# Performance work log

Measured on AMD Instinct MI355X. Metric: run time of the kernel, lower is better.

The kernel has to match this reference:

```python
import jax, jax.numpy as jnp
import numpy as np
from functools import partial

DIM, HID, DK, NH, SEQ, B = 1024, 512, 512, 4, 16, 2048
DH = DK // NH  # per-head dim = 128
EPS = 1e-5


def _ln(x, g, b):
    m = x.mean(-1, keepdims=True)
    v = ((x - m) ** 2).mean(-1, keepdims=True)
    return (x - m) * jax.lax.rsqrt(v + EPS) * g + b


def setup_inputs() -> dict:
    key = jax.random.key(0)
    ks = jax.random.split(key, 32)
    it = iter(range(32))
    n = lambda shape, s: jax.random.normal(ks[next(it)], shape, jnp.float32) * s
    inp = {
        'visual': n((B, SEQ, DIM), 1.0),
        'text':   n((B, SEQ, DIM), 1.0),
        'user':   n((B, SEQ, DIM), 1.0),
        'cat':    n((B, SEQ, DIM), 1.0),
        'label':  n((B, SEQ, 1), 1.0),
        'h0':     n((B, HID), 1.0),
        'c0':     n((B, HID), 1.0),
        # fusion MLP: Linear(4*dim -> dim)
        'fus_W': n((DIM, 4 * DIM), 1.0 / np.sqrt(4 * DIM)),
        'fus_b': n((DIM,), 0.01),
        # LayerNormLSTM cell params (gate order i,f,g,o)
        'W_ih': n((4 * HID, DIM), 1.0 / np.sqrt(DIM)),
        'W_hh': n((4 * HID, HID), 1.0 / np.sqrt(HID)),
        'g_ih': 1.0 + n((4 * HID,), 0.1), 'b_ih': n((4 * HID,), 0.01),
        'g_hh': 1.0 + n((4 * HID,), 0.1), 'b_hh': n((4 * HID,), 0.01),
        'g_c':  1.0 + n((HID,), 0.1),     'b_c':  n((HID,), 0.01),
        # attention projections
        'wq_W': n((DK, HID), 1.0 / np.sqrt(HID)), 'wq_b': n((DK,), 0.01),
        'wk_W': n((DK, HID), 1.0 / np.sqrt(HID)), 'wk_b': n((DK,), 0.01),
        'wv_W': n((NH, DK, HID), 1.0 / np.sqrt(HID)), 'wv_b': n((NH, DK), 0.01),
        'wout_W': n((DK, DK * NH), 1.0 / np.sqrt(DK * NH)), 'wout_b': n((DK,), 0.01),
        'out_W': n((1, DK), 1.0 / np.sqrt(DK)), 'out_b': n((1,), 0.01),
    }
    return inp


def reference(visual, text, user, cat, label, h0, c0, fus_W, fus_b,
              W_ih, W_hh, g_ih, b_ih, g_hh, b_hh, g_c, b_c,
              wq_W, wq_b, wk_W, wk_b, wv_W, wv_b, wout_W, wout_b, out_W, out_b):
    # fusion MLP (dropout is identity at inference)
    mods = jnp.concatenate([visual, text, user, cat], axis=-1)  # [B,S,4*DIM]
    v_t = jax.nn.relu(mods @ fus_W.T + fus_b)                    # [B,S,DIM]

    # LayerNorm-LSTM recurrence over time via scan
    def step(carry, x_t):
        h, c = carry
        gates = _ln(x_t @ W_ih.T, g_ih, b_ih) + _ln(h @ W_hh.T, g_hh, b_hh)
        i, f, g, o = jnp.split(gates, 4, axis=-1)
        c = jax.nn.sigmoid(f) * c + jax.nn.sigmoid(i) * jnp.tanh(g)
        h = jax.nn.sigmoid(o) * jnp.tanh(_ln(c, g_c, b_c))
        return (h, c), h

    (hn, _), hs = jax.lax.scan(step, (h0, c0), jnp.swapaxes(v_t, 0, 1))
    lstm_out = jnp.swapaxes(hs, 0, 1)  # [B,S,HID]

    # multi-head dot self-attention against final hidden state
    q = (hn @ wq_W.T + wq_b).reshape(-1, NH, DH)                    # [B,H,dh]
    k = (lstm_out @ wk_W.T + wk_b).reshape(-1, SEQ, NH, DH)         # [B,S,H,dh]
    scores = jnp.einsum('bshd,bhd->bhs', k, q) / np.sqrt(DH)        # [B,H,S]
    attn = jax.nn.softmax(scores, axis=-1)
    # per-head full-width values: V[b,h,s,k]
    V = jnp.einsum('hkd,bsd->bhsk', wv_W, lstm_out) + wv_b[None, :, None, :]
    ctx = jnp.einsum('bhsk,bhs->bhk', V, attn).reshape(-1, NH * DK)  # [B,H*DK]
    out_h = ctx @ wout_W.T + wout_b                                  # [B,DK]
    output = out_h @ out_W.T + out_b                                 # [B,1]

    label_one = label[:, -1, 0]
    loss = jnp.mean((output.reshape(-1) - label_one) ** 2)
    return loss, output
```

## Files before the change

kernel.cpp:

```cpp
#include <hip/hip_runtime.h>
#include <cstdint>

#define B_SZ 2048
#define SEQ  16
#define DIM  1024
#define HID  512
#define DK   512
#define NH   4
#define DH   128
#define GATE 2048
#define EPSV 1e-5f

typedef __bf16 bf8_t __attribute__((ext_vector_type(8)));
typedef float  f4_t  __attribute__((ext_vector_type(4)));
typedef unsigned short u16x8 __attribute__((ext_vector_type(8)));
typedef unsigned short u16x4 __attribute__((ext_vector_type(4)));

__device__ __forceinline__ unsigned short f2bf(float f){
  __bf16 h = (__bf16)f;
  return __builtin_bit_cast(unsigned short, h);
}
__device__ __forceinline__ float bf2f(unsigned short u){
  return __builtin_bit_cast(float, ((unsigned int)u) << 16);
}
__device__ __forceinline__ float sigm(float x){ return 1.f/(1.f+__expf(-x)); }
__device__ __forceinline__ float tanh_f(float x){ return 1.f - 2.f/(__expf(2.f*x)+1.f); }

__device__ __forceinline__ void gload16(const void* g, void* l){
  __builtin_amdgcn_global_load_lds(
      (const __attribute__((address_space(1))) void*)g,
      (__attribute__((address_space(3))) void*)l, 16, 0, 0);
}

template<bool OUT_BF16, bool BIAS, bool RELU>
__global__ __launch_bounds__(256) void gemm16(
    const unsigned short* __restrict__ A,
    const unsigned short* __restrict__ Bw,
    const float* __restrict__ bias,
    void* __restrict__ Cp,
    int N, int K, int nwg)
{
  __shared__ __align__(16) unsigned short As[128*64];
  __shared__ __align__(16) unsigned short Bs[128*64];
  const int tid = threadIdx.x, lane = tid & 63, wave = tid >> 6;
  const int bid = blockIdx.x;
  const int swz = (bid & 7)*(nwg >> 3) + (bid >> 3);
  const int nx  = N >> 7;
  const int lnx = 31 - __clz(nx);
  const int bm0 = (swz >> lnx) << 7;
  const int bn0 = (swz & (nx-1)) << 7;

  const int r8  = lane >> 3;
  const int gsw = ((lane & 7) ^ r8) * 8;
  const unsigned short* Ab = A  + (size_t)(bm0 + wave*32 + r8)*K + gsw;
  const unsigned short* Bb = Bw + (size_t)(bn0 + wave*32 + r8)*K + gsw;
  unsigned short* la = As + wave*2048;
  unsigned short* lb = Bs + wave*2048;

  f4_t acc[4][4];
  #pragma unroll
  for (int m=0;m<4;++m)
    #pragma unroll
    for (int n=0;n<4;++n) acc[m][n] = (f4_t)0.f;

  const int KT = K >> 6;
  const int fr = lane & 15, kg = lane >> 4;
  const int wm = (wave & 1)*64, wn = (wave >> 1)*64;

  for (int kt = 0; kt < KT; ++kt){
    if (kt) __syncthreads();
    const size_t ko = (size_t)kt*64;
    #pragma unroll
    for (int q = 0; q < 4; ++q){
      gload16(Ab + ko + (size_t)q*8*K, la + q*512);
      gload16(Bb + ko + (size_t)q*8*K, lb + q*512);
    }
    __syncthreads();
    #pragma unroll
    for (int kk = 0; kk < 2; ++kk){
      bf8_t af[4], bf_[4];
      #pragma unroll
      for (int m=0;m<4;++m){
        const int r = wm+m*16+fr;
        af[m]  = *(const bf8_t*)&As[r*64 + (((kk*4+kg) ^ (r&7))*8)];
      }
      #pragma unroll
      for (int n=0;n<4;++n){
        const int r = wn+n*16+fr;
        bf_[n] = *(const bf8_t*)&Bs[r*64 + (((kk*4+kg) ^ (r&7))*8)];
      }
      #pragma unroll
      for (int m=0;m<4;++m)
        #pragma unroll
        for (int n=0;n<4;++n)
          acc[m][n] = __builtin_amdgcn_mfma_f32_16x16x32_bf16(af[m], bf_[n], acc[m][n], 0,0,0);
    }
  }

  #pragma unroll
  for (int n=0;n<4;++n){
    const int col = bn0 + wn + n*16 + fr;
    float bv = 0.f;
    if constexpr (BIAS) bv = bias[col];
    #pragma unroll
    for (int m=0;m<4;++m){
      #pragma unroll
      for (int j=0;j<4;++j){
        const int row = bm0 + wm + m*16 + kg*4 + j;
        float v = acc[m][n][j] + bv;
        if constexpr (RELU) v = fmaxf(v, 0.f);
        if constexpr (OUT_BF16) ((unsigned short*)Cp)[(size_t)row*N + col] = f2bf(v);
        else                    ((float*)Cp)[(size_t)row*N + col] = v;
      }
    }
  }
}

template<bool OUT_BF16, bool BIAS>
__global__ __launch_bounds__(256) void gemm64(
    const unsigned short* __restrict__ A,
    const unsigned short* __restrict__ Bw,
    const float* __restrict__ bias,
    void* __restrict__ Cp,
    int N, int K, int nwg)
{
  __shared__ __align__(16) unsigned short As[64*64];
  __shared__ __align__(16) unsigned short Bs[64*64];
  const int tid = threadIdx.x, lane = tid & 63, wave = tid >> 6;
  const int bid = blockIdx.x;
  const int swz = (bid & 7)*(nwg >> 3) + (bid >> 3);
  const int nx  = N >> 6;
  const int lnx = 31 - __clz(nx);
  const int bm0 = (swz >> lnx) << 6;
  const int bn0 = (swz & (nx-1)) << 6;

  const int r8  = lane >> 3;
  const int gsw = ((lane & 7) ^ r8) * 8;
  const unsigned short* Ab = A  + (size_t)(bm0 + wave*16 + r8)*K + gsw;
  const unsigned short* Bb = Bw + (size_t)(bn0 + wave*16 + r8)*K + gsw;
  unsigned short* la = As + wave*1024;
  unsigned short* lb = Bs + wave*1024;

  f4_t acc[2][2];
  #pragma unroll
  for (int m=0;m<2;++m)
    #pragma unroll
    for (int n=0;n<2;++n) acc[m][n] = (f4_t)0.f;

  const int KT = K >> 6;
  const int fr = lane & 15, kg = lane >> 4;
  const int wm = (wave & 1)*32, wn = (wave >> 1)*32;

  for (int kt = 0; kt < KT; ++kt){
    if (kt) __syncthreads();
    const size_t ko = (size_t)kt*64;
    #pragma unroll
    for (int q = 0; q < 2; ++q){
      gload16(Ab + ko + (size_t)q*8*K, la + q*512);
      gload16(Bb + ko + (size_t)q*8*K, lb + q*512);
    }
    __syncthreads();
    #pragma unroll
    for (int kk = 0; kk < 2; ++kk){
      bf8_t af[2], bf_[2];
      #pragma unroll
      for (int m=0;m<2;++m){
        const int r = wm+m*16+fr;
        af[m]  = *(const bf8_t*)&As[r*64 + (((kk*4+kg) ^ (r&7))*8)];
      }
      #pragma unroll
      for (int n=0;n<2;++n){
        const int r = wn+n*16+fr;
        bf_[n] = *(const bf8_t*)&Bs[r*64 + (((kk*4+kg) ^ (r&7))*8)];
      }
      #pragma unroll
      for (int m=0;m<2;++m)
        #pragma unroll
        for (int n=0;n<2;++n)
          acc[m][n] = __builtin_amdgcn_mfma_f32_16x16x32_bf16(af[m], bf_[n], acc[m][n], 0,0,0);
    }
  }

  #pragma unroll
  for (int n=0;n<2;++n){
    const int col = bn0 + wn + n*16 + fr;
    float bv = 0.f;
    if constexpr (BIAS) bv = bias[col];
    #pragma unroll
    for (int m=0;m<2;++m){
      #pragma unroll
      for (int j=0;j<4;++j){
        const int row = bm0 + wm + m*16 + kg*4 + j;
        float v = acc[m][n][j] + bv;
        if constexpr (OUT_BF16) ((unsigned short*)Cp)[(size_t)row*N + col] = f2bf(v);
        else                    ((float*)Cp)[(size_t)row*N + col] = v;
      }
    }
  }
}

__global__ __launch_bounds__(256) void lstm_step(
  const unsigned short* __restrict__ X, const unsigned short* __restrict__ Gh,
  const float* __restrict__ c_src, float* __restrict__ c_dst,
  const float* __restrict__ g_ih, const float* __restrict__ b_ih,
  const float* __restrict__ g_hh, const float* __restrict__ b_hh,
  const float* __restrict__ g_c,  const float* __restrict__ b_c,
  unsigned short* __restrict__ h_out, unsigned short* __restrict__ lstm_out,
  int t)
{
  const int b = blockIdx.x, tid = threadIdx.x;
  __shared__ float xs[GATE];
  __shared__ float gs[GATE];
  __shared__ float red[32];
  const unsigned short* xrow = X  + ((size_t)b*SEQ + t)*GATE;
  const unsigned short* grow = Gh + (size_t)b*GATE;
  u16x8 xv = *(const u16x8*)&xrow[tid*8];
  u16x8 gv = *(const u16x8*)&grow[tid*8];
  float sx=0,sx2=0,sg=0,sg2=0;
  #pragma unroll
  for (int j=0;j<8;++j){
    float x = bf2f(xv[j]), g = bf2f(gv[j]);
    xs[tid*8+j]=x; gs[tid*8+j]=g;
    sx += x; sx2 += x*x; sg += g; sg2 += g*g;
  }
  #pragma unroll
  for (int m=32;m;m>>=1){
    sx += __shfl_xor(sx,m); sx2 += __shfl_xor(sx2,m);
    sg += __shfl_xor(sg,m); sg2 += __shfl_xor(sg2,m);
  }
  const int w = tid>>6;
  if ((tid&63)==0){ red[w]=sx; red[4+w]=sx2; red[8+w]=sg; red[12+w]=sg2; }
  __syncthreads();
  sx  = red[0]+red[1]+red[2]+red[3];
  sx2 = red[4]+red[5]+red[6]+red[7];
  sg  = red[8]+red[9]+red[10]+red[11];
  sg2 = red[12]+red[13]+red[14]+red[15];
  const float mX = sx*(1.f/GATE), mH = sg*(1.f/GATE);
  const float rX = rsqrtf(sx2*(1.f/GATE)-mX*mX+EPSV);
  const float rH = rsqrtf(sg2*(1.f/GATE)-mH*mH+EPSV);

  float cN[2], xo[2]; float sc=0, sc2=0;
  #pragma unroll
  for (int rep=0;rep<2;++rep){
    const int n = tid + rep*256;
    const int ni=n, nf=n+HID, ng=n+2*HID, no=n+3*HID;
    float gi = (xs[ni]-mX)*rX*g_ih[ni]+b_ih[ni] + (gs[ni]-mH)*rH*g_hh[ni]+b_hh[ni];
    float gf = (xs[nf]-mX)*rX*g_ih[nf]+b_ih[nf] + (gs[nf]-mH)*rH*g_hh[nf]+b_hh[nf];
    float gg = (xs[ng]-mX)*rX*g_ih[ng]+b_ih[ng] + (gs[ng]-mH)*rH*g_hh[ng]+b_hh[ng];
    float go = (xs[no]-mX)*rX*g_ih[no]+b_ih[no] + (gs[no]-mH)*rH*g_hh[no]+b_hh[no];
    float co = c_src[(size_t)b*HID + n];
    float cn = sigm(gf)*co + sigm(gi)*tanh_f(gg);
    cN[rep]=cn; xo[rep]=go;
    sc += cn; sc2 += cn*cn;
  }
  #pragma unroll
  for (int m=32;m;m>>=1){ sc += __shfl_xor(sc,m); sc2 += __shfl_xor(sc2,m); }
  if ((tid&63)==0){ red[16+w]=sc; red[20+w]=sc2; }
  __syncthreads();
  sc  = red[16]+red[17]+red[18]+red[19];
  sc2 = red[20]+red[21]+red[22]+red[23];
  const float mC = sc*(1.f/HID);
  const float rC = rsqrtf(sc2*(1.f/HID)-mC*mC+EPSV);
  #pragma unroll
  for (int rep=0;rep<2;++rep){
    const int n = tid + rep*256;
    float hN = sigm(xo[rep])*tanh_f((cN[rep]-mC)*rC*g_c[n]+b_c[n]);
    c_dst[(size_t)b*HID+n] = cN[rep];
    unsigned short hbv = f2bf(hN);
    h_out[(size_t)b*HID+n] = hbv;
    lstm_out[((size_t)b*SEQ+t)*HID+n] = hbv;
  }
}

__global__ __launch_bounds__(256) void attn_out_k(
  const float* __restrict__ q, const unsigned short* __restrict__ Km,
  const unsigned short* __restrict__ lo_all,
  const float* __restrict__ u, const float* __restrict__ Cc,
  float* __restrict__ out)
{
  const int b = blockIdx.x, tid = threadIdx.x;
  __shared__ float qs[DK];
  __shared__ float sc[NH][SEQ];
  __shared__ float at[NH][SEQ];
  __shared__ float red[4];
  for (int i=tid; i<DK; i+=256) qs[i] = q[(size_t)b*DK + i];
  __syncthreads();
  {
    const int p = tid>>2, sub = tid&3, h = p>>4, s = p&15;
    const unsigned short* krow = Km + ((size_t)b*SEQ + s)*DK + h*DH + sub*32;
    const float* qh = &qs[h*DH + sub*32];
    float part = 0.f;
    #pragma unroll
    for (int c8=0;c8<4;++c8){
      u16x8 kv = *(const u16x8*)(krow + c8*8);
      #pragma unroll
      for (int j=0;j<8;++j) part += qh[c8*8+j]*bf2f(kv[j]);
    }
    part += __shfl_xor(part,1); part += __shfl_xor(part,2);
    if (sub==0) sc[h][s] = part * 0.08838834764831845f;
  }
  __syncthreads();
  if (tid < 64){
    const int h = tid>>4;
    float v = sc[h][tid&15], mx = v;
    #pragma unroll
    for (int m=1;m<16;m<<=1) mx = fmaxf(mx, __shfl_xor(mx,m));
    float e = __expf(v-mx), se = e;
    #pragma unroll
    for (int m=1;m<16;m<<=1) se += __shfl_xor(se,m);
    at[h][tid&15] = e/se;
  }
  __syncthreads();
  float accum = 0.f;
  #pragma unroll
  for (int it=0; it<4; ++it){
    const int idx = it*256 + tid;
    const int h = idx>>8, d0 = (idx&255)*2;
    const unsigned short* lo = lo_all + (size_t)b*SEQ*HID + d0;
    float p0=0.f, p1=0.f;
    #pragma unroll
    for (int s=0;s<16;++s){
      unsigned int pr = *(const unsigned int*)(lo + s*HID);
      float a = at[h][s];
      p0 += a*bf2f((unsigned short)(pr&0xffffu));
      p1 += a*bf2f((unsigned short)(pr>>16));
    }
    accum += u[h*HID+d0]*p0 + u[h*HID+d0+1]*p1;
  }
  #pragma unroll
  for (int m=32;m;m>>=1) accum += __shfl_xor(accum,m);
  if ((tid&63)==0) red[tid>>6] = accum;
  __syncthreads();
  if (tid==0) out[1+b] = red[0]+red[1]+red[2]+red[3] + Cc[0];
}

__global__ __launch_bounds__(256) void loss_k(const float* __restrict__ label, float* __restrict__ out){
  const int tid = threadIdx.x;
  __shared__ float red[4];
  float s = 0.f;
  for (int b=tid; b<B_SZ; b+=256){
    float d = out[1+b] - label[(size_t)b*SEQ + (SEQ-1)];
    s += d*d;
  }
  #pragma unroll
  for (int m=32;m;m>>=1) s += __shfl_xor(s,m);
  if ((tid&63)==0) red[tid>>6]=s;
  __syncthreads();
  if (tid==0) out[0] = (red[0]+red[1]+red[2]+red[3]) * (1.f/B_SZ);
}

__global__ __launch_bounds__(256) void cvt_bf16_k(const float* __restrict__ in, unsigned short* __restrict__ o, int n){
  int i = (blockIdx.x*256 + threadIdx.x)*4;
  if (i < n){
    f4_t v = *(const f4_t*)&in[i];
    u16x4 w;
    #pragma unroll
    for (int j=0;j<4;++j) w[j] = f2bf(v[j]);
    *(u16x4*)&o[i] = w;
  }
}

__global__ __launch_bounds__(256) void cvt4_k(
  const float* __restrict__ v0, const float* __restrict__ v1,
  const float* __restrict__ v2, const float* __restrict__ v3,
  unsigned short* __restrict__ dst)
{
  const int idx = blockIdx.x*256 + threadIdx.x;
  const int src = blockIdx.y;
  const float* s = src==0?v0 : src==1?v1 : src==2?v2 : v3;
  const size_t e0 = (size_t)idx*8;
  const int row = (int)(e0 >> 10);
  const int col = (int)(e0 & 1023);
  f4_t a = *(const f4_t*)&s[e0];
  f4_t b = *(const f4_t*)&s[e0+4];
  u16x8 w;
  #pragma unroll
  for (int j=0;j<4;++j){ w[j]=f2bf(a[j]); w[4+j]=f2bf(b[j]); }
  *(u16x8*)&dst[(size_t)row*4096 + src*1024 + col] = w;
}

__global__ __launch_bounds__(256) void fold_we_k(
  const float* __restrict__ wout_W, const float* __restrict__ out_W, float* __restrict__ we)
{
  const int j = blockIdx.x*256 + threadIdx.x;
  float s=0.f;
  for (int m=0;m<512;++m) s += out_W[m]*wout_W[(size_t)m*2048+j];
  we[j]=s;
}
__global__ __launch_bounds__(256) void fold_u_k(
  const float* __restrict__ we, const float* __restrict__ wv_W, float* __restrict__ u)
{
  const int o = blockIdx.x*256 + threadIdx.x;
  const int h = o>>9, d = o&511;
  const float* wv = wv_W + (size_t)h*262144 + d;
  const float* wp = we + h*512;
  float s=0.f;
  for (int k=0;k<512;++k) s += wp[k]*wv[(size_t)k*512];
  u[o]=s;
}
__global__ __launch_bounds__(256) void fold_c_k(
  const float* __restrict__ we, const float* __restrict__ wv_b,
  const float* __restrict__ out_W, const float* __restrict__ wout_b,
  const float* __restrict__ out_b, float* __restrict__ Cc)
{
  const int tid = threadIdx.x;
  __shared__ float red[4];
  float s=0.f;
  for (int j=tid;j<2048;j+=256) s += we[j]*wv_b[j];
  for (int m=tid;m<512;m+=256)  s += out_W[m]*wout_b[m];
  #pragma unroll
  for (int m=32;m;m>>=1) s += __shfl_xor(s,m);
  if ((tid&63)==0) red[tid>>6]=s;
  __syncthreads();
  if (tid==0) Cc[0] = red[0]+red[1]+red[2]+red[3] + out_b[0];
}

extern "C" void kernel_launch(void* const* d_in, const int* in_sizes, int n_in,
                              void* d_out, int out_size, void* d_ws, size_t ws_size,
                              hipStream_t stream)
{
  const float* visual = (const float*)d_in[0];
  const float* text   = (const float*)d_in[1];
  const float* user_  = (const float*)d_in[2];
  const float* cat_   = (const float*)d_in[3];
  const float* label  = (const float*)d_in[4];
  const float* h0     = (const float*)d_in[5];
  const float* c0     = (const float*)d_in[6];
  const float* fus_W  = (const float*)d_in[7];
  const float* fus_b  = (const float*)d_in[8];
  const float* W_ih   = (const float*)d_in[9];
  const float* W_hh   = (const float*)d_in[10];
  const float* g_ih   = (const float*)d_in[11];
  const float* b_ih   = (const float*)d_in[12];
  const float* g_hh   = (const float*)d_in[13];
  const float* b_hh   = (const float*)d_in[14];
  const float* g_c    = (const float*)d_in[15];
  const float* b_c    = (const float*)d_in[16];
  const float* wq_W   = (const float*)d_in[17];
  const float* wq_b   = (const float*)d_in[18];
  const float* wk_W   = (const float*)d_in[19];
  const float* wk_b   = (const float*)d_in[20];
  const float* wv_W   = (const float*)d_in[21];
  const float* wv_b   = (const float*)d_in[22];
  const float* wout_W = (const float*)d_in[23];
  const float* wout_b = (const float*)d_in[24];
  const float* out_W  = (const float*)d_in[25];
  const float* out_b  = (const float*)d_in[26];
  (void)in_sizes; (void)n_in; (void)out_size; (void)ws_size;

  char* base = (char*)d_ws; size_t off = 0;
  auto alloc = [&](size_t n)->void*{ void* p = base+off; off += n; off = (off+255)&~(size_t)255; return p; };
  unsigned short* modsB = (unsigned short*)alloc((size_t)32768*4096*2);
  unsigned short* X     = modsB;
  unsigned short* vt    = (unsigned short*)alloc((size_t)32768*1024*2);
  unsigned short* Gh    = (unsigned short*)alloc((size_t)2048*2048*2);
  float*          cws   = (float*)         alloc((size_t)2048*512*4);
  unsigned short* hb    = (unsigned short*)alloc((size_t)2048*512*2);
  unsigned short* lo    = (unsigned short*)alloc((size_t)32768*512*2);
  unsigned short* Km    = (unsigned short*)alloc((size_t)32768*512*2);
  float*          qb    = (float*)         alloc((size_t)2048*512*4);
  unsigned short* fusWb = (unsigned short*)alloc((size_t)1024*4096*2);
  unsigned short* Wihb  = (unsigned short*)alloc((size_t)2048*1024*2);
  unsigned short* Whhb  = (unsigned short*)alloc((size_t)2048*512*2);
  unsigned short* wqb   = (unsigned short*)alloc((size_t)512*512*2);
  unsigned short* wkb   = (unsigned short*)alloc((size_t)512*512*2);
  float*          we_ws = (float*)         alloc(2048*4);
  float*          u_ws  = (float*)         alloc(2048*4);
  float*          C_ws  = (float*)         alloc(256);

  cvt4_k<<<dim3(16384,4), dim3(256), 0, stream>>>(visual, text, user_, cat_, modsB);
  cvt_bf16_k<<<dim3(4096), dim3(256), 0, stream>>>(fus_W, fusWb, 1024*4096);
  cvt_bf16_k<<<dim3(2048), dim3(256), 0, stream>>>(W_ih,  Wihb,  2048*1024);
  cvt_bf16_k<<<dim3(1024), dim3(256), 0, stream>>>(W_hh,  Whhb,  2048*512);
  cvt_bf16_k<<<dim3(256),  dim3(256), 0, stream>>>(wq_W,  wqb,   512*512);
  cvt_bf16_k<<<dim3(256),  dim3(256), 0, stream>>>(wk_W,  wkb,   512*512);
  cvt_bf16_k<<<dim3(1024), dim3(256), 0, stream>>>(h0,    hb,    2048*512);
  fold_we_k<<<dim3(8), dim3(256), 0, stream>>>(wout_W, out_W, we_ws);
  fold_u_k <<<dim3(8), dim3(256), 0, stream>>>(we_ws, wv_W, u_ws);
  fold_c_k <<<dim3(1), dim3(256), 0, stream>>>(we_ws, wv_b, out_W, wout_b, out_b, C_ws);

  gemm16<true,true,true><<<dim3(2048), dim3(256), 0, stream>>>(
      modsB, fusWb, fus_b, vt, 1024, 4096, 2048);
  gemm16<true,false,false><<<dim3(4096), dim3(256), 0, stream>>>(
      vt, Wihb, nullptr, X, 2048, 1024, 4096);

  for (int t=0; t<SEQ; ++t){
    gemm64<true,false><<<dim3(1024), dim3(256), 0, stream>>>(
        hb, Whhb, nullptr, Gh, 2048, 512, 1024);
    lstm_step<<<dim3(2048), dim3(256), 0, stream>>>(
        X, Gh, (t==0 ? c0 : cws), cws, g_ih, b_ih, g_hh, b_hh, g_c, b_c, hb, lo, t);
  }

  gemm64<false,true><<<dim3(256), dim3(256), 0, stream>>>(
      hb, wqb, wq_b, qb, 512, 512, 256);
  gemm16<true,true,false><<<dim3(1024), dim3(256), 0, stream>>>(
      lo, wkb, wk_b, Km, 512, 512, 1024);

  attn_out_k<<<dim3(2048), dim3(256), 0, stream>>>(qb, Km, lo, u_ws, C_ws, (float*)d_out);
  loss_k<<<dim3(1), dim3(256), 0, stream>>>(label, (float*)d_out);
}
```

Baseline: 1.039 ms.

## Replace 128x128 GEMM with double-buffered 256x256 tile kernel using 8 waves

The large input-projection GEMMs move from a 128x128, 4-wave kernel to a 256x256, 8-wave kernel with double-buffered LDS staging and explicit vmcnt waits, so global loads overlap MFMA work. The bigger tile raises operand reuse per LDS load. MFMA blocks also get raised scheduling priority. This uses 128KB of LDS per block, which limits occupancy to one block per CU, and gives fewer workgroups for the smaller Km GEMM.

```diff
diff --git a/kernel.cpp b/kernel.cpp
--- a/kernel.cpp
+++ b/kernel.cpp
@@ -33,80 +33,100 @@
 }
 
 template<bool OUT_BF16, bool BIAS, bool RELU>
-__global__ __launch_bounds__(256) void gemm16(
+__global__ __launch_bounds__(512, 2) void gemm256(
     const unsigned short* __restrict__ A,
     const unsigned short* __restrict__ Bw,
     const float* __restrict__ bias,
     void* __restrict__ Cp,
     int N, int K, int nwg)
 {
-  __shared__ __align__(16) unsigned short As[128*64];
-  __shared__ __align__(16) unsigned short Bs[128*64];
-  const int tid = threadIdx.x, lane = tid & 63, wave = tid >> 6;
+  __shared__ __align__(16) unsigned short As[2][256*64];
+  __shared__ __align__(16) unsigned short Bs[2][256*64];
+  const int tid = threadIdx.x, lane = tid & 63, w = tid >> 6;
   const int bid = blockIdx.x;
   const int swz = (bid & 7)*(nwg >> 3) + (bid >> 3);
-  const int nx  = N >> 7;
+  const int nx  = N >> 8;
   const int lnx = 31 - __clz(nx);
-  const int bm0 = (swz >> lnx) << 7;
-  const int bn0 = (swz & (nx-1)) << 7;
+  const int bm0 = (swz >> lnx) << 8;
+  const int bn0 = (swz & (nx-1)) << 8;
 
   const int r8  = lane >> 3;
   const int gsw = ((lane & 7) ^ r8) * 8;
-  const unsigned short* Ab = A  + (size_t)(bm0 + wave*32 + r8)*K + gsw;
-  const unsigned short* Bb = Bw + (size_t)(bn0 + wave*32 + r8)*K + gsw;
-  unsigned short* la = As + wave*2048;
-  unsigned short* lb = Bs + wave*2048;
-
-  f4_t acc[4][4];
-  #pragma unroll
-  for (int m=0;m<4;++m)
+  const unsigned short* Ab = A  + (size_t)(bm0 + w*32 + r8)*K + gsw;
+  const unsigned short* Bb = Bw + (size_t)(bn0 + w*32 + r8)*K + gsw;
+
+  f4_t acc[8][4];
+  #pragma unroll
+  for (int m=0;m<8;++m)
     #pragma unroll
     for (int n=0;n<4;++n) acc[m][n] = (f4_t)0.f;
 
+  const int fr = lane & 15, kg = lane >> 4;
+  const int ra0 = (w & 1)*128, rb0 = (w >> 1)*64;
   const int KT = K >> 6;
-  const int fr = lane & 15, kg = lane >> 4;
-  const int wm = (wave & 1)*64, wn = (wave >> 1)*64;
-
-  for (int kt = 0; kt < KT; ++kt){
-    if (kt) __syncthreads();
+
+  auto stage = [&](int buf, int kt){
     const size_t ko = (size_t)kt*64;
     #pragma unroll
-    for (int q = 0; q < 4; ++q){
-      gload16(Ab + ko + (size_t)q*8*K, la + q*512);
-      gload16(Bb + ko + (size_t)q*8*K, lb + q*512);
-    }
-    __syncthreads();
-    #pragma unroll
-    for (int kk = 0; kk < 2; ++kk){
-      bf8_t af[4], bf_[4];
-      #pragma unroll
-      for (int m=0;m<4;++m){
-        const int r = wm+m*16+fr;
-        af[m]  = *(const bf8_t*)&As[r*64 + (((kk*4+kg) ^ (r&7))*8)];
+    for (int q=0;q<4;++q){
+      gload16(Ab + ko + (size_t)q*8*K, &As[buf][(w*4+q)*512]);
+      gload16(Bb + ko + (size_t)q*8*K, &Bs[buf][(w*4+q)*512]);
+    }
+  };
+
+  stage(0, 0);
+  for (int kt=0; kt<KT; ++kt){
+    const int cur = kt & 1;
+    __builtin_amdgcn_sched_barrier(0);
+    if (kt+1 < KT){
+      stage(cur^1, kt+1);
+      asm volatile("s_waitcnt vmcnt(8)" ::: "memory");
+    } else {
+      asm volatile("s_waitcnt vmcnt(0)" ::: "memory");
+    }
+    __builtin_amdgcn_s_barrier();
+    bf8_t bfr[4][2];
+    #pragma unroll
+    for (int n=0;n<4;++n)
+      #pragma unroll
+      for (int kk=0;kk<2;++kk){
+        const int r = rb0 + n*16 + fr;
+        bfr[n][kk] = *(const bf8_t*)&Bs[cur][r*64 + (((kk*4+kg) ^ (r&7))*8)];
       }
-      #pragma unroll
-      for (int n=0;n<4;++n){
-        const int r = wn+n*16+fr;
-        bf_[n] = *(const bf8_t*)&Bs[r*64 + (((kk*4+kg) ^ (r&7))*8)];
-      }
-      #pragma unroll
-      for (int m=0;m<4;++m)
+    #pragma unroll
+    for (int half=0; half<2; ++half){
+      bf8_t af[4][2];
+      #pragma unroll
+      for (int mi=0;mi<4;++mi)
+        #pragma unroll
+        for (int kk=0;kk<2;++kk){
+          const int r = ra0 + (half*4+mi)*16 + fr;
+          af[mi][kk] = *(const bf8_t*)&As[cur][r*64 + (((kk*4+kg) ^ (r&7))*8)];
+        }
+      __builtin_amdgcn_s_setprio(1);
+      #pragma unroll
+      for (int mi=0;mi<4;++mi)
         #pragma unroll
         for (int n=0;n<4;++n)
-          acc[m][n] = __builtin_amdgcn_mfma_f32_16x16x32_bf16(af[m], bf_[n], acc[m][n], 0,0,0);
-    }
+          #pragma unroll
+          for (int kk=0;kk<2;++kk)
+            acc[half*4+mi][n] = __builtin_amdgcn_mfma_f32_16x16x32_bf16(
+                af[mi][kk], bfr[n][kk], acc[half*4+mi][n], 0,0,0);
+      __builtin_amdgcn_s_setprio(0);
+    }
+    __builtin_amdgcn_s_barrier();
   }
 
   #pragma unroll
   for (int n=0;n<4;++n){
-    const int col = bn0 + wn + n*16 + fr;
+    const int col = bn0 + rb0 + n*16 + fr;
     float bv = 0.f;
     if constexpr (BIAS) bv = bias[col];
     #pragma unroll
-    for (int m=0;m<4;++m){
+    for (int m=0;m<8;++m){
       #pragma unroll
       for (int j=0;j<4;++j){
-        const int row = bm0 + wm + m*16 + kg*4 + j;
+        const int row = bm0 + ra0 + m*16 + kg*4 + j;
         float v = acc[m][n][j] + bv;
         if constexpr (RELU) v = fmaxf(v, 0.f);
         if constexpr (OUT_BF16) ((unsigned short*)Cp)[(size_t)row*N + col] = f2bf(v);
@@ -479,10 +499,10 @@
   fold_u_k <<<dim3(8), dim3(256), 0, stream>>>(we_ws, wv_W, u_ws);
   fold_c_k <<<dim3(1), dim3(256), 0, stream>>>(we_ws, wv_b, out_W, wout_b, out_b, C_ws);
 
-  gemm16<true,true,true><<<dim3(2048), dim3(256), 0, stream>>>(
-      modsB, fusWb, fus_b, vt, 1024, 4096, 2048);
-  gemm16<true,false,false><<<dim3(4096), dim3(256), 0, stream>>>(
-      vt, Wihb, nullptr, X, 2048, 1024, 4096);
+  gemm256<true,true,true><<<dim3(512), dim3(512), 0, stream>>>(
+      modsB, fusWb, fus_b, vt, 1024, 4096, 512);
+  gemm256<true,false,false><<<dim3(1024), dim3(512), 0, stream>>>(
+      vt, Wihb, nullptr, X, 2048, 1024, 1024);
 
   for (int t=0; t<SEQ; ++t){
     gemm64<true,false><<<dim3(1024), dim3(256), 0, stream>>>(
@@ -493,8 +513,8 @@
 
   gemm64<false,true><<<dim3(256), dim3(256), 0, stream>>>(
       hb, wqb, wq_b, qb, 512, 512, 256);
-  gemm16<true,true,false><<<dim3(1024), dim3(256), 0, stream>>>(
-      lo, wkb, wk_b, Km, 512, 512, 1024);
+  gemm256<true,true,false><<<dim3(256), dim3(512), 0, stream>>>(
+      lo, wkb, wk_b, Km, 512, 512, 256);
 
   attn_out_k<<<dim3(2048), dim3(256), 0, stream>>>(qb, Km, lo, u_ws, C_ws, (float*)d_out);
   loss_k<<<dim3(1), dim3(256), 0, stream>>>(label, (float*)d_out);
```

New measurement: 1.080 ms. +4.0%, slower.

## Fuse LSTM recurrence into one persistent kernel and fold input conversion into fusion GEMM

Applied to the files above, without the earlier changes.

Replaces the 32 per-timestep launches (h·W_hh GEMM plus LSTM cell kernel) with a single kernel in which each block owns 16 batch rows for all timesteps. It keeps h in LDS and c in registers, computes the recurrent GEMM with MFMA reading W_hh straight from global memory, and applies the LayerNorms in place. The fusion GEMM now reads the four fp32 modality inputs directly and converts them to bf16 while staging them in LDS, which removes the separate concat/convert kernel and its large intermediate buffer. The trade-off is that only 128 blocks run the recurrence, so occupancy is low, and every block re-reads W_hh from global or cache each step.

```diff
diff --git a/kernel.cpp b/kernel.cpp
--- a/kernel.cpp
+++ b/kernel.cpp
@@ -10,6 +10,7 @@
 #define DH   128
 #define GATE 2048
 #define EPSV 1e-5f
+#define RROWS 16
 
 typedef __bf16 bf8_t __attribute__((ext_vector_type(8)));
 typedef float  f4_t  __attribute__((ext_vector_type(4)));
@@ -116,6 +117,120 @@
   }
 }
 
+__global__ __launch_bounds__(256) void gemm16f(
+    const float* __restrict__ A0, const float* __restrict__ A1,
+    const float* __restrict__ A2, const float* __restrict__ A3,
+    const unsigned short* __restrict__ Bw,
+    const float* __restrict__ bias,
+    unsigned short* __restrict__ Cp,
+    int N, int K, int nwg)
+{
+  __shared__ __align__(16) unsigned short As[128*64];
+  __shared__ __align__(16) unsigned short Bs[128*64];
+  const int tid = threadIdx.x, lane = tid & 63, wave = tid >> 6;
+  const int bid = blockIdx.x;
+  const int swz = (bid & 7)*(nwg >> 3) + (bid >> 3);
+  const int nx  = N >> 7;
+  const int lnx = 31 - __clz(nx);
+  const int bm0 = (swz >> lnx) << 7;
+  const int bn0 = (swz & (nx-1)) << 7;
+
+  const int r8  = lane >> 3;
+  const int gsw = ((lane & 7) ^ r8) * 8;
+  const unsigned short* Bb = Bw + (size_t)(bn0 + wave*32 + r8)*K + gsw;
+  unsigned short* lb = Bs + wave*2048;
+
+  const int arow = tid >> 3, acolg = tid & 7;
+  f4_t ra[4][2];
+
+  auto loadA = [&](int kt){
+    const int kbase = kt*64;
+    const int src = kbase >> 10;
+    const int kc  = kbase & 1023;
+    const float* Asel = src==0?A0 : src==1?A1 : src==2?A2 : A3;
+    #pragma unroll
+    for (int q=0;q<4;++q){
+      const float* p = Asel + (size_t)(bm0 + q*32 + arow)*1024 + kc + acolg*8;
+      ra[q][0] = *(const f4_t*)p;
+      ra[q][1] = *(const f4_t*)(p+4);
+    }
+  };
+  auto storeA = [&](){
+    #pragma unroll
+    for (int q=0;q<4;++q){
+      const int row = q*32 + arow;
+      u16x8 wv;
+      #pragma unroll
+      for (int j=0;j<4;++j){ wv[j]=f2bf(ra[q][0][j]); wv[4+j]=f2bf(ra[q][1][j]); }
+      *(u16x8*)&As[row*64 + ((acolg ^ (row&7))*8)] = wv;
+    }
+  };
+
+  f4_t acc[4][4];
+  #pragma unroll
+  for (int m=0;m<4;++m)
+    #pragma unroll
+    for (int n=0;n<4;++n) acc[m][n] = (f4_t)0.f;
+
+  const int KT = K >> 6;
+  const int fr = lane & 15, kg = lane >> 4;
+  const int wm = (wave & 1)*64, wn = (wave >> 1)*64;
+
+  loadA(0);
+  for (int kt = 0; kt < KT; ++kt){
+    if (kt) __builtin_amdgcn_s_barrier();
+    storeA();
+    const size_t ko = (size_t)kt*64;
+    #pragma unroll
+    for (int q = 0; q < 4; ++q) gload16(Bb + ko + (size_t)q*8*K, lb + q*512);
+    __builtin_amdgcn_sched_barrier(0);
+    if (kt+1 < KT){
+      loadA(kt+1);
+      __builtin_amdgcn_sched_barrier(0);
+      asm volatile("s_waitcnt vmcnt(8)" ::: "memory");
+    } else {
+      asm volatile("s_waitcnt vmcnt(0)" ::: "memory");
+    }
+    asm volatile("s_waitcnt lgkmcnt(0)" ::: "memory");
+    __builtin_amdgcn_s_barrier();
+    __builtin_amdgcn_sched_barrier(0);
+    #pragma unroll
+    for (int kk = 0; kk < 2; ++kk){
+      bf8_t af[4], bf_[4];
+      #pragma unroll
+      for (int m=0;m<4;++m){
+        const int r = wm+m*16+fr;
+        af[m]  = *(const bf8_t*)&As[r*64 + (((kk*4+kg) ^ (r&7))*8)];
+      }
+      #pragma unroll
+      for (int n=0;n<4;++n){
+        const int r = wn+n*16+fr;
+        bf_[n] = *(const bf8_t*)&Bs[r*64 + (((kk*4+kg) ^ (r&7))*8)];
+      }
+      #pragma unroll
+      for (int m=0;m<4;++m)
+        #pragma unroll
+        for (int n=0;n<4;++n)
+          acc[m][n] = __builtin_amdgcn_mfma_f32_16x16x32_bf16(af[m], bf_[n], acc[m][n], 0,0,0);
+    }
+  }
+
+  #pragma unroll
+  for (int n=0;n<4;++n){
+    const int col = bn0 + wn + n*16 + fr;
+    const float bv = bias[col];
+    #pragma unroll
+    for (int m=0;m<4;++m){
+      #pragma unroll
+      for (int j=0;j<4;++j){
+        const int row = bm0 + wm + m*16 + kg*4 + j;
+        float v = fmaxf(acc[m][n][j] + bv, 0.f);
+        Cp[(size_t)row*N + col] = f2bf(v);
+      }
+    }
+  }
+}
+
 template<bool OUT_BF16, bool BIAS>
 __global__ __launch_bounds__(256) void gemm64(
     const unsigned short* __restrict__ A,
@@ -199,76 +314,156 @@
   }
 }
 
-__global__ __launch_bounds__(256) void lstm_step(
-  const unsigned short* __restrict__ X, const unsigned short* __restrict__ Gh,
-  const float* __restrict__ c_src, float* __restrict__ c_dst,
+__global__ __launch_bounds__(512) void rec_fused(
+  const unsigned short* __restrict__ X,
+  const unsigned short* __restrict__ Whhb,
+  const float* __restrict__ h0, const float* __restrict__ c0,
   const float* __restrict__ g_ih, const float* __restrict__ b_ih,
   const float* __restrict__ g_hh, const float* __restrict__ b_hh,
   const float* __restrict__ g_c,  const float* __restrict__ b_c,
-  unsigned short* __restrict__ h_out, unsigned short* __restrict__ lstm_out,
-  int t)
-{
-  const int b = blockIdx.x, tid = threadIdx.x;
-  __shared__ float xs[GATE];
-  __shared__ float gs[GATE];
-  __shared__ float red[32];
-  const unsigned short* xrow = X  + ((size_t)b*SEQ + t)*GATE;
-  const unsigned short* grow = Gh + (size_t)b*GATE;
-  u16x8 xv = *(const u16x8*)&xrow[tid*8];
-  u16x8 gv = *(const u16x8*)&grow[tid*8];
-  float sx=0,sx2=0,sg=0,sg2=0;
-  #pragma unroll
-  for (int j=0;j<8;++j){
-    float x = bf2f(xv[j]), g = bf2f(gv[j]);
-    xs[tid*8+j]=x; gs[tid*8+j]=g;
-    sx += x; sx2 += x*x; sg += g; sg2 += g*g;
-  }
-  #pragma unroll
-  for (int m=32;m;m>>=1){
-    sx += __shfl_xor(sx,m); sx2 += __shfl_xor(sx2,m);
-    sg += __shfl_xor(sg,m); sg2 += __shfl_xor(sg2,m);
-  }
-  const int w = tid>>6;
-  if ((tid&63)==0){ red[w]=sx; red[4+w]=sx2; red[8+w]=sg; red[12+w]=sg2; }
+  unsigned short* __restrict__ lo,
+  unsigned short* __restrict__ hb)
+{
+  __shared__ float gates[RROWS*2048];
+  __shared__ unsigned short hsh[RROWS*512];
+  __shared__ float part[8][RROWS][2];
+  __shared__ float stats[RROWS][4];
+  const int tid = threadIdx.x, lane = tid & 63, w = tid >> 6;
+  const int r0  = blockIdx.x * RROWS;
+  const int fr  = lane & 15, kg = lane >> 4;
+  const int erow = tid >> 5, el = tid & 31;
+
+  float c_reg[16];
+  #pragma unroll
+  for (int q4=0;q4<4;++q4){
+    const int col0 = el*4 + q4*128;
+    f4_t hv = *(const f4_t*)&h0[(size_t)(r0+erow)*HID + col0];
+    u16x4 hw;
+    #pragma unroll
+    for (int j=0;j<4;++j) hw[j] = f2bf(hv[j]);
+    const int g16 = (col0 >> 3) ^ (erow & 7);
+    *(u16x4*)&hsh[erow*512 + (g16<<3) + (col0 & 7)] = hw;
+    f4_t cv = *(const f4_t*)&c0[(size_t)(r0+erow)*HID + col0];
+    #pragma unroll
+    for (int j=0;j<4;++j) c_reg[q4*4+j] = cv[j];
+  }
   __syncthreads();
-  sx  = red[0]+red[1]+red[2]+red[3];
-  sx2 = red[4]+red[5]+red[6]+red[7];
-  sg  = red[8]+red[9]+red[10]+red[11];
-  sg2 = red[12]+red[13]+red[14]+red[15];
-  const float mX = sx*(1.f/GATE), mH = sg*(1.f/GATE);
-  const float rX = rsqrtf(sx2*(1.f/GATE)-mX*mX+EPSV);
-  const float rH = rsqrtf(sg2*(1.f/GATE)-mH*mH+EPSV);
-
-  float cN[2], xo[2]; float sc=0, sc2=0;
-  #pragma unroll
-  for (int rep=0;rep<2;++rep){
-    const int n = tid + rep*256;
-    const int ni=n, nf=n+HID, ng=n+2*HID, no=n+3*HID;
-    float gi = (xs[ni]-mX)*rX*g_ih[ni]+b_ih[ni] + (gs[ni]-mH)*rH*g_hh[ni]+b_hh[ni];
-    float gf = (xs[nf]-mX)*rX*g_ih[nf]+b_ih[nf] + (gs[nf]-mH)*rH*g_hh[nf]+b_hh[nf];
-    float gg = (xs[ng]-mX)*rX*g_ih[ng]+b_ih[ng] + (gs[ng]-mH)*rH*g_hh[ng]+b_hh[ng];
-    float go = (xs[no]-mX)*rX*g_ih[no]+b_ih[no] + (gs[no]-mH)*rH*g_hh[no]+b_hh[no];
-    float co = c_src[(size_t)b*HID + n];
-    float cn = sigm(gf)*co + sigm(gi)*tanh_f(gg);
-    cN[rep]=cn; xo[rep]=go;
-    sc += cn; sc2 += cn*cn;
-  }
-  #pragma unroll
-  for (int m=32;m;m>>=1){ sc += __shfl_xor(sc,m); sc2 += __shfl_xor(sc2,m); }
-  if ((tid&63)==0){ red[16+w]=sc; red[20+w]=sc2; }
-  __syncthreads();
-  sc  = red[16]+red[17]+red[18]+red[19];
-  sc2 = red[20]+red[21]+red[22]+red[23];
-  const float mC = sc*(1.f/HID);
-  const float rC = rsqrtf(sc2*(1.f/HID)-mC*mC+EPSV);
-  #pragma unroll
-  for (int rep=0;rep<2;++rep){
-    const int n = tid + rep*256;
-    float hN = sigm(xo[rep])*tanh_f((cN[rep]-mC)*rC*g_c[n]+b_c[n]);
-    c_dst[(size_t)b*HID+n] = cN[rep];
-    unsigned short hbv = f2bf(hN);
-    h_out[(size_t)b*HID+n] = hbv;
-    lstm_out[((size_t)b*SEQ+t)*HID+n] = hbv;
+
+  for (int t=0; t<SEQ; ++t){
+    f4_t acc[16];
+    #pragma unroll
+    for (int n=0;n<16;++n) acc[n] = (f4_t)0.f;
+    #pragma unroll 2
+    for (int kt=0; kt<16; ++kt){
+      bf8_t af = *(const bf8_t*)&hsh[fr*512 + (((kt*4+kg) ^ (fr&7))*8)];
+      #pragma unroll
+      for (int n=0;n<16;++n){
+        const int col = w*256 + n*16 + fr;
+        bf8_t bf_ = *(const bf8_t*)&Whhb[(size_t)col*HID + kt*32 + kg*8];
+        acc[n] = __builtin_amdgcn_mfma_f32_16x16x32_bf16(af, bf_, acc[n], 0,0,0);
+      }
+    }
+    float ps[4], ps2[4];
+    #pragma unroll
+    for (int j=0;j<4;++j){ ps[j]=0.f; ps2[j]=0.f; }
+    #pragma unroll
+    for (int n=0;n<16;++n){
+      const int col = w*256 + n*16 + fr;
+      #pragma unroll
+      for (int j=0;j<4;++j){
+        const int row = kg*4 + j;
+        const float v = acc[n][j];
+        gates[row*2048 + ((((col>>2) ^ (row&7))<<2) | (col&3))] = v;
+        ps[j] += v; ps2[j] += v*v;
+      }
+    }
+    #pragma unroll
+    for (int m=1;m<16;m<<=1){
+      #pragma unroll
+      for (int j=0;j<4;++j){ ps[j]+=__shfl_xor(ps[j],m); ps2[j]+=__shfl_xor(ps2[j],m); }
+    }
+    if (fr==0){
+      #pragma unroll
+      for (int j=0;j<4;++j){ part[w][kg*4+j][0]=ps[j]; part[w][kg*4+j][1]=ps2[j]; }
+    }
+    u16x4 xq[4][4];
+    float sx=0.f, sx2=0.f;
+    const unsigned short* xrow = X + ((size_t)(r0+erow)*SEQ + t)*GATE;
+    #pragma unroll
+    for (int q4=0;q4<4;++q4){
+      const int hid0 = el*4 + q4*128;
+      #pragma unroll
+      for (int qd=0;qd<4;++qd){
+        xq[q4][qd] = *(const u16x4*)(xrow + qd*HID + hid0);
+        #pragma unroll
+        for (int j=0;j<4;++j){ float x = bf2f(xq[q4][qd][j]); sx+=x; sx2+=x*x; }
+      }
+    }
+    #pragma unroll
+    for (int m=1;m<32;m<<=1){ sx+=__shfl_xor(sx,m); sx2+=__shfl_xor(sx2,m); }
+    if (el==0){
+      const float mX = sx*(1.f/GATE);
+      stats[erow][2]=mX; stats[erow][3]=rsqrtf(sx2*(1.f/GATE)-mX*mX+EPSV);
+    }
+    __syncthreads();
+    if (tid < RROWS){
+      float s=0.f, s2=0.f;
+      #pragma unroll
+      for (int ww=0;ww<8;++ww){ s+=part[ww][tid][0]; s2+=part[ww][tid][1]; }
+      const float mH = s*(1.f/GATE);
+      stats[tid][0]=mH; stats[tid][1]=rsqrtf(s2*(1.f/GATE)-mH*mH+EPSV);
+    }
+    __syncthreads();
+    const float mH=stats[erow][0], rH=stats[erow][1];
+    const float mX=stats[erow][2], rX=stats[erow][3];
+    float go_s[16], cs=0.f, cs2=0.f;
+    #pragma unroll
+    for (int q4=0;q4<4;++q4){
+      const int hid0 = el*4 + q4*128;
+      const int gswz = (erow&7);
+      const f4_t ghi = *(const f4_t*)&gates[erow*2048 + ((((hid0     )>>2) ^ gswz)<<2)];
+      const f4_t ghf = *(const f4_t*)&gates[erow*2048 + ((((hid0+ 512)>>2) ^ gswz)<<2)];
+      const f4_t ghg = *(const f4_t*)&gates[erow*2048 + ((((hid0+1024)>>2) ^ gswz)<<2)];
+      const f4_t gho = *(const f4_t*)&gates[erow*2048 + ((((hid0+1536)>>2) ^ gswz)<<2)];
+      const f4_t gi1=*(const f4_t*)&g_ih[hid0],      bi1=*(const f4_t*)&b_ih[hid0];
+      const f4_t gi2=*(const f4_t*)&g_ih[hid0+512],  bi2=*(const f4_t*)&b_ih[hid0+512];
+      const f4_t gi3=*(const f4_t*)&g_ih[hid0+1024], bi3=*(const f4_t*)&b_ih[hid0+1024];
+      const f4_t gi4=*(const f4_t*)&g_ih[hid0+1536], bi4=*(const f4_t*)&b_ih[hid0+1536];
+      const f4_t gh1=*(const f4_t*)&g_hh[hid0],      bh1=*(const f4_t*)&b_hh[hid0];
+      const f4_t gh2=*(const f4_t*)&g_hh[hid0+512],  bh2=*(const f4_t*)&b_hh[hid0+512];
+      const f4_t gh3=*(const f4_t*)&g_hh[hid0+1024], bh3=*(const f4_t*)&b_hh[hid0+1024];
+      const f4_t gh4=*(const f4_t*)&g_hh[hid0+1536], bh4=*(const f4_t*)&b_hh[hid0+1536];
+      #pragma unroll
+      for (int j=0;j<4;++j){
+        float gi = (bf2f(xq[q4][0][j])-mX)*rX*gi1[j]+bi1[j] + (ghi[j]-mH)*rH*gh1[j]+bh1[j];
+        float gf = (bf2f(xq[q4][1][j])-mX)*rX*gi2[j]+bi2[j] + (ghf[j]-mH)*rH*gh2[j]+bh2[j];
+        float gg = (bf2f(xq[q4][2][j])-mX)*rX*gi3[j]+bi3[j] + (ghg[j]-mH)*rH*gh3[j]+bh3[j];
+        float go = (bf2f(xq[q4][3][j])-mX)*rX*gi4[j]+bi4[j] + (gho[j]-mH)*rH*gh4[j]+bh4[j];
+        const float cn = sigm(gf)*c_reg[q4*4+j] + sigm(gi)*tanh_f(gg);
+        c_reg[q4*4+j] = cn; go_s[q4*4+j] = go;
+        cs += cn; cs2 += cn*cn;
+      }
+    }
+    #pragma unroll
+    for (int m=1;m<32;m<<=1){ cs+=__shfl_xor(cs,m); cs2+=__shfl_xor(cs2,m); }
+    const float mC = cs*(1.f/HID);
+    const float rC = rsqrtf(cs2*(1.f/HID)-mC*mC+EPSV);
+    #pragma unroll
+    for (int q4=0;q4<4;++q4){
+      const int hid0 = el*4 + q4*128;
+      const f4_t gc4=*(const f4_t*)&g_c[hid0], bc4=*(const f4_t*)&b_c[hid0];
+      u16x4 hw;
+      #pragma unroll
+      for (int j=0;j<4;++j){
+        float hN = sigm(go_s[q4*4+j])*tanh_f((c_reg[q4*4+j]-mC)*rC*gc4[j]+bc4[j]);
+        hw[j] = f2bf(hN);
+      }
+      const int g16 = (hid0 >> 3) ^ (erow & 7);
+      *(u16x4*)&hsh[erow*512 + (g16<<3) + (hid0 & 7)] = hw;
+      *(u16x4*)&lo[((size_t)(r0+erow)*SEQ + t)*HID + hid0] = hw;
+      if (t==SEQ-1) *(u16x4*)&hb[(size_t)(r0+erow)*HID + hid0] = hw;
+    }
+    __syncthreads();
   }
 }
 
@@ -358,25 +553,6 @@
     for (int j=0;j<4;++j) w[j] = f2bf(v[j]);
     *(u16x4*)&o[i] = w;
   }
-}
-
-__global__ __launch_bounds__(256) void cvt4_k(
-  const float* __restrict__ v0, const float* __restrict__ v1,
-  const float* __restrict__ v2, const float* __restrict__ v3,
-  unsigned short* __restrict__ dst)
-{
-  const int idx = blockIdx.x*256 + threadIdx.x;
-  const int src = blockIdx.y;
-  const float* s = src==0?v0 : src==1?v1 : src==2?v2 : v3;
-  const size_t e0 = (size_t)idx*8;
-  const int row = (int)(e0 >> 10);
-  const int col = (int)(e0 & 1023);
-  f4_t a = *(const f4_t*)&s[e0];
-  f4_t b = *(const f4_t*)&s[e0+4];
-  u16x8 w;
-  #pragma unroll
-  for (int j=0;j<4;++j){ w[j]=f2bf(a[j]); w[4+j]=f2bf(b[j]); }
-  *(u16x8*)&dst[(size_t)row*4096 + src*1024 + col] = w;
 }
 
 __global__ __launch_bounds__(256) void fold_we_k(
@@ -450,14 +626,11 @@
 
   char* base = (char*)d_ws; size_t off = 0;
   auto alloc = [&](size_t n)->void*{ void* p = base+off; off += n; off = (off+255)&~(size_t)255; return p; };
-  unsigned short* modsB = (unsigned short*)alloc((size_t)32768*4096*2);
-  unsigned short* X     = modsB;
+  unsigned short* X     = (unsigned short*)alloc((size_t)32768*2048*2);
   unsigned short* vt    = (unsigned short*)alloc((size_t)32768*1024*2);
-  unsigned short* Gh    = (unsigned short*)alloc((size_t)2048*2048*2);
-  float*          cws   = (float*)         alloc((size_t)2048*512*4);
-  unsigned short* hb    = (unsigned short*)alloc((size_t)2048*512*2);
   unsigned short* lo    = (unsigned short*)alloc((size_t)32768*512*2);
   unsigned short* Km    = (unsigned short*)alloc((size_t)32768*512*2);
+  unsigned short* hb    = (unsigned short*)alloc((size_t)2048*512*2);
   float*          qb    = (float*)         alloc((size_t)2048*512*4);
   unsigned short* fusWb = (unsigned short*)alloc((size_t)1024*4096*2);
   unsigned short* Wihb  = (unsigned short*)alloc((size_t)2048*1024*2);
@@ -468,28 +641,22 @@
   float*          u_ws  = (float*)         alloc(2048*4);
   float*          C_ws  = (float*)         alloc(256);
 
-  cvt4_k<<<dim3(16384,4), dim3(256), 0, stream>>>(visual, text, user_, cat_, modsB);
   cvt_bf16_k<<<dim3(4096), dim3(256), 0, stream>>>(fus_W, fusWb, 1024*4096);
   cvt_bf16_k<<<dim3(2048), dim3(256), 0, stream>>>(W_ih,  Wihb,  2048*1024);
   cvt_bf16_k<<<dim3(1024), dim3(256), 0, stream>>>(W_hh,  Whhb,  2048*512);
   cvt_bf16_k<<<dim3(256),  dim3(256), 0, stream>>>(wq_W,  wqb,   512*512);
   cvt_bf16_k<<<dim3(256),  dim3(256), 0, stream>>>(wk_W,  wkb,   512*512);
-  cvt_bf16_k<<<dim3(1024), dim3(256), 0, stream>>>(h0,    hb,    2048*512);
   fold_we_k<<<dim3(8), dim3(256), 0, stream>>>(wout_W, out_W, we_ws);
   fold_u_k <<<dim3(8), dim3(256), 0, stream>>>(we_ws, wv_W, u_ws);
   fold_c_k <<<dim3(1), dim3(256), 0, stream>>>(we_ws, wv_b, out_W, wout_b, out_b, C_ws);
 
-  gemm16<true,true,true><<<dim3(2048), dim3(256), 0, stream>>>(
-      modsB, fusWb, fus_b, vt, 1024, 4096, 2048);
+  gemm16f<<<dim3(2048), dim3(256), 0, stream>>>(
+      visual, text, user_, cat_, fusWb, fus_b, vt, 1024, 4096, 2048);
   gemm16<true,false,false><<<dim3(4096), dim3(256), 0, stream>>>(
       vt, Wihb, nullptr, X, 2048, 1024, 4096);
 
-  for (int t=0; t<SEQ; ++t){
-    gemm64<true,false><<<dim3(1024), dim3(256), 0, stream>>>(
-        hb, Whhb, nullptr, Gh, 2048, 512, 1024);
-    lstm_step<<<dim3(2048), dim3(256), 0, stream>>>(
-        X, Gh, (t==0 ? c0 : cws), cws, g_ih, b_ih, g_hh, b_hh, g_c, b_c, hb, lo, t);
-  }
+  rec_fused<<<dim3(128), dim3(512), 0, stream>>>(
+      X, Whhb, h0, c0, g_ih, b_ih, g_hh, b_hh, g_c, b_c, lo, hb);
 
   gemm64<false,true><<<dim3(256), dim3(256), 0, stream>>>(
       hb, wqb, wq_b, qb, 512, 512, 256);
```

Result: slower. 2.571 ms (+147.5%).
